# Performance work log

Hardware: AMD Instinct MI355X
Metric: run time of the kernel (lower is better)

Reference implementation:

```python
import jax, jax.numpy as jnp
import numpy as np
from jax import lax

EPS = 1e-10

def _ln(x, g, b):
    m = x.mean(-1, keepdims=True)
    v = x.var(-1, keepdims=True)
    return (x - m) / jnp.sqrt(v + 1e-5) * g + b

def _gather(t, idx):
    # t: (B, HW, c), idx: (B, HW, d) -> (B, HW, d, c); out[n,i,k,:] = t[n, idx[n,i,k], :]
    return jax.vmap(lambda tn, In: tn[In])(t, idx)

def setup_inputs() -> dict:
    key = jax.random.key(0)
    ks = jax.random.split(key, 20)
    b, v, c, d, h, w, hid, ksz = 2, 2, 128, 64, 64, 64, 256, 5
    hw = h * w
    Bf = b * v  # v_1 == 1 target view per reference view
    std = 0.02
    return {
        'features_mv': jax.random.normal(ks[0], (b, v, c, h, w), jnp.float32),
        'warp_indices': jax.random.randint(ks[1], (Bf, hw, d), 0, hw, jnp.int32),
        'depth_prob': jax.random.uniform(ks[2], (Bf, hw, d), jnp.float32),
        'ln1_g': jnp.ones((c,), jnp.float32), 'ln1_b': jnp.zeros((c,), jnp.float32),
        'wq': jax.random.normal(ks[3], (c, c), jnp.float32) * std, 'bq': jnp.zeros((c,), jnp.float32),
        'wk': jax.random.normal(ks[4], (c, c), jnp.float32) * std, 'bk': jnp.zeros((c,), jnp.float32),
        'wv': jax.random.normal(ks[5], (c, c), jnp.float32) * std, 'bv': jnp.zeros((c,), jnp.float32),
        'k_pe': jax.random.normal(ks[6], (1, 1, d), jnp.float32) * std,
        'v_pe': jax.random.normal(ks[7], (1, 1, d), jnp.float32) * std,
        'rpe': jax.random.normal(ks[8], (1, 1, d), jnp.float32) * std,
        'proj_w': jax.random.normal(ks[9], (c, c), jnp.float32) * std, 'proj_b': jnp.zeros((c,), jnp.float32),
        'ln2_g': jnp.ones((c,), jnp.float32), 'ln2_b': jnp.zeros((c,), jnp.float32),
        'fc1_w': jax.random.normal(ks[10], (c, hid), jnp.float32) * std, 'fc1_b': jnp.zeros((hid,), jnp.float32),
        'dw_w': jax.random.normal(ks[11], (hid, 1, ksz, ksz), jnp.float32) * std, 'dw_b': jnp.zeros((hid,), jnp.float32),
        'fc2_w': jax.random.normal(ks[12], (hid, c), jnp.float32) * std, 'fc2_b': jnp.zeros((c,), jnp.float32),
    }

def reference(features_mv, warp_indices, depth_prob, ln1_g, ln1_b, wq, bq, wk, bk, wv, bv,
              k_pe, v_pe, rpe, proj_w, proj_b, ln2_g, ln2_b, fc1_w, fc1_b, dw_w, dw_b, fc2_w, fc2_b):
    b, v, c, h, w = features_mv.shape
    hw = h * w
    hid = fc1_w.shape[1]
    scale = c ** (-0.5)  # num_heads = 1 -> head_dim = dim

    # (b v) (h w) c
    x = features_mv.reshape(b * v, c, hw).transpose(0, 2, 1)
    shortcut = x
    xn = _ln(x, ln1_g, ln1_b)
    q = xn @ wq + bq
    k = xn @ wk + bk
    vv = xn @ wv + bv

    # nn pairing: v=2, v_1=1 -> each reference view attends the other view
    Q = (q.reshape(b, v, hw, c) * scale).reshape(b * v, hw, c)
    K = k.reshape(b, v, hw, c)[:, ::-1].reshape(b * v, hw, c)
    V = vv.reshape(b, v, hw, c)[:, ::-1].reshape(b * v, hw, c)

    # SMM_QmK: cost[n,i,k] = sum_c Q[n,i,c] * K[n, idx[n,i,k], c]
    Kg = _gather(K, warp_indices)                       # (B, hw, d, c)
    cost = jnp.einsum('bic,bikc->bik', Q, Kg)
    Q_pe = Q.sum(-1, keepdims=True)                     # (B, hw, 1)
    cost = cost + Q_pe * k_pe + rpe                     # broadcast (1,1,d)

    # (Sim_UNet similarity refinement omitted: UNetModel source unavailable; identity here)
    attn = jax.nn.softmax(cost, axis=-1)
    attn = attn * depth_prob
    attn = (attn + EPS) / (attn.sum(-1, keepdims=True) + EPS)

    # SMM_AmV: out[n,i,c] = sum_k attn[n,i,k] * V[n, idx[n,i,k], c]
    Vg = _gather(V, warp_indices)                       # (B, hw, d, c)
    out = jnp.einsum('bik,bikc->bic', attn, Vg)
    out = out + (attn * v_pe).sum(-1, keepdims=True)

    # projection + residual (v_1 == 1 so B == b*v)
    x = shortcut + (out @ proj_w + proj_b)

    # ConvFFN residual branch
    xn2 = _ln(x, ln2_g, ln2_b)
    y = jax.nn.gelu(xn2 @ fc1_w + fc1_b, approximate=False)
    yi = y.transpose(0, 2, 1).reshape(b * v, hid, h, w)
    yc = lax.conv_general_dilated(yi, dw_w, (1, 1), 'SAME', feature_group_count=hid,
                                  dimension_numbers=('NCHW', 'OIHW', 'NCHW'))
    yc = jax.nn.gelu(yc + dw_b[None, :, None, None], approximate=False)
    y = y + yc.reshape(b * v, hid, hw).transpose(0, 2, 1)
    y = y @ fc2_w + fc2_b
    return x + y
```

## Files before the change

### kernel.cpp

```cpp
#include <hip/hip_runtime.h>
#include <math.h>

#define TOK   16384
#define HW    4096
#define C     128
#define D     64
#define HID   256

constexpr float LN_EPS = 1e-5f;
constexpr float EPS_R  = 1e-10f;
constexpr float QSCALE = 0.08838834764831845f;

typedef __attribute__((ext_vector_type(8))) short  bf16x8;
typedef __attribute__((ext_vector_type(4))) float  f32x4;
typedef __attribute__((ext_vector_type(2))) _Float16 half2v;
#define MFMA16(a, b, c) __builtin_amdgcn_mfma_f32_16x16x32_bf16((a), (b), (c), 0, 0, 0)

__device__ __forceinline__ float bflo(unsigned u) { return __uint_as_float(u << 16); }
__device__ __forceinline__ float bfhi(unsigned u) { return __uint_as_float(u & 0xffff0000u); }
__device__ __forceinline__ float bfu(unsigned short u) { return __uint_as_float((unsigned)u << 16); }
__device__ __forceinline__ unsigned short f2bf(float f) {
  unsigned u = __float_as_uint(f);
  unsigned r = (u + 0x7fffu + ((u >> 16) & 1u)) >> 16;
  return (unsigned short)r;
}
__device__ __forceinline__ unsigned short f2h(float f) {
  _Float16 h = (_Float16)f;
  unsigned short r;
  __builtin_memcpy(&r, &h, 2);
  return r;
}
__device__ __forceinline__ float gelu_exact(float x) {
  return 0.5f * x * (1.0f + erff(x * 0.7071067811865476f));
}

union U4H { uint4 v; half2v h[4]; };
union U1H { unsigned v; half2v h; };

#if __has_builtin(__builtin_amdgcn_fdot2)
__device__ __forceinline__ float dot2h(half2v a, half2v b, float c) {
  return __builtin_amdgcn_fdot2(a, b, c, false);
}
#else
__device__ __forceinline__ float dot2h(half2v a, half2v b, float c) {
  return c + (float)a.x * (float)b.x + (float)a.y * (float)b.y;
}
#endif

__global__ __launch_bounds__(256) void k_prepln1(const float* __restrict__ wq,
    const float* __restrict__ wk, const float* __restrict__ wv,
    const float* __restrict__ pw, const float* __restrict__ f1w,
    const float* __restrict__ f2w, unsigned short* __restrict__ wt,
    const float* __restrict__ feat, const float* __restrict__ g,
    const float* __restrict__ b, unsigned short* __restrict__ xnb) {
  __shared__ float tile[32][C + 1];
  int bidx = blockIdx.x;
  if (bidx < 512) {
    int id = bidx * 256 + threadIdx.x;
    if (id < 16384) {
      int n = id >> 7, k = id & 127;
      wt[id] = f2bf(wq[k * 128 + n]);
    } else if (id < 32768) {
      int e = id - 16384; int n = e >> 7, k = e & 127;
      wt[id] = f2bf(wk[k * 128 + n]);
    } else if (id < 49152) {
      int e = id - 32768; int n = e >> 7, k = e & 127;
      wt[id] = f2bf(wv[k * 128 + n]);
    } else if (id < 65536) {
      int e = id - 49152; int n = e >> 7, k = e & 127;
      wt[id] = f2bf(pw[k * 128 + n]);
    } else if (id < 98304) {
      int e = id - 65536; int n = e >> 7, k = e & 127;
      wt[id] = f2bf(f1w[k * 256 + n]);
    } else {
      int e = id - 98304; int n = e >> 8, k = e & 255;
      wt[id] = f2bf(f2w[k * 128 + n]);
    }
    return;
  }
  int t0 = (bidx - 512) * 32;
  int n = t0 / HW, i0 = t0 % HW;
  int tid = threadIdx.x;
  const float* fb = feat + (size_t)n * C * HW;
  for (int e = tid; e < 32 * C; e += 256) {
    int ch = e >> 5, ii = e & 31;
    tile[ii][ch] = fb[(size_t)ch * HW + i0 + ii];
  }
  __syncthreads();
  int wave = tid >> 6, lane = tid & 63;
  for (int tkn = wave; tkn < 32; tkn += 4) {
    float a0 = tile[tkn][lane];
    float a1 = tile[tkn][lane + 64];
    float s = a0 + a1;
    for (int off = 32; off; off >>= 1) s += __shfl_xor(s, off, 64);
    float mean = s * (1.0f / 128.0f);
    float d0 = a0 - mean, d1 = a1 - mean;
    float v = d0 * d0 + d1 * d1;
    for (int off = 32; off; off >>= 1) v += __shfl_xor(v, off, 64);
    float rstd = rsqrtf(v * (1.0f / 128.0f) + LN_EPS);
    size_t ro = (size_t)(t0 + tkn) * C;
    xnb[ro + lane]      = f2bf(d0 * rstd * g[lane] + b[lane]);
    xnb[ro + lane + 64] = f2bf(d1 * rstd * g[lane + 64] + b[lane + 64]);
  }
}

__global__ __launch_bounds__(256) void k_qkv(const unsigned short* __restrict__ xnb,
    const unsigned short* __restrict__ wt,
    const float* __restrict__ bq, const float* __restrict__ bk,
    const float* __restrict__ bv, unsigned short* __restrict__ qh,
    unsigned short* __restrict__ ksw, unsigned short* __restrict__ vsw) {
  int w = threadIdx.x >> 6, lane = threadIdx.x & 63;
  int q4 = lane >> 4, m = lane & 15;
  int t0 = blockIdx.x * 64 + w * 16;
  int wsel = blockIdx.y >> 1;
  int hf = blockIdx.y & 1;
  const unsigned short* Wt = wt + wsel * 16384;
  const unsigned short* ap = xnb + (size_t)(t0 + m) * C + q4 * 8;
  bf16x8 a[4];
  #pragma unroll
  for (int ks = 0; ks < 4; ks++) a[ks] = *(const bf16x8*)(ap + ks * 32);
  f32x4 acc[4];
  #pragma unroll
  for (int nt = 0; nt < 4; nt++) acc[nt] = (f32x4){0.f, 0.f, 0.f, 0.f};
  #pragma unroll
  for (int nt = 0; nt < 4; nt++) {
    const unsigned short* bp = Wt + (size_t)(hf * 64 + nt * 16 + m) * C + q4 * 8;
    #pragma unroll
    for (int ks = 0; ks < 4; ks++) {
      bf16x8 bfrag = *(const bf16x8*)(bp + ks * 32);
      acc[nt] = MFMA16(a[ks], bfrag, acc[nt]);
    }
  }
  const float* B = (wsel == 0) ? bq : ((wsel == 1) ? bk : bv);
  float sc = (wsel == 0) ? QSCALE : 1.0f;
  unsigned short* O = (wsel == 0) ? qh : ((wsel == 1) ? ksw : vsw);
  int n = t0 >> 12, i0 = t0 & 4095;
  int base = (wsel == 0) ? t0 : (((n ^ 1) << 12) + i0);
  #pragma unroll
  for (int nt = 0; nt < 4; nt++) {
    int col = hf * 64 + nt * 16 + m;
    float bb = B[col];
    #pragma unroll
    for (int reg = 0; reg < 4; reg++) {
      int row = base + q4 * 4 + reg;
      O[(size_t)row * C + col] = f2h((acc[nt][reg] + bb) * sc);
    }
  }
}

__global__ __launch_bounds__(256) void k_attn(const unsigned short* __restrict__ qh,
    const unsigned short* __restrict__ ksw, const unsigned short* __restrict__ vsw,
    const int* __restrict__ widx, const float* __restrict__ dprob,
    const float* __restrict__ kpe, const float* __restrict__ vpe,
    const float* __restrict__ rpe, unsigned short* __restrict__ aoutb) {
  int lane = threadIdx.x & 63;
  int wave = threadIdx.x >> 6;
  int bid = blockIdx.x;
  int n = (bid >> 1) & 3;
  int within = ((bid >> 3) << 1) | (bid & 1);
  int token = n * HW + within * 4 + wave;
  const unsigned short* Kb = ksw + (size_t)n * HW * C;
  const unsigned short* Vb = vsw + (size_t)n * HW * C;
  int g = lane >> 3, s = lane & 7;
  int myidx = widx[(size_t)token * D + lane];
  float mydp = dprob[(size_t)token * D + lane];
  half2v qreg[8];
  {
    const unsigned short* qp = qh + (size_t)token * C + s * 16;
    U4H qa, qb2;
    qa.v = *(const uint4*)(qp);
    qb2.v = *(const uint4*)(qp + 8);
    #pragma unroll
    for (int i = 0; i < 4; i++) { qreg[i] = qa.h[i]; qreg[4 + i] = qb2.h[i]; }
  }
  half2v ones = {(_Float16)1.0f, (_Float16)1.0f};
  float qpe = 0.f;
  #pragma unroll
  for (int i = 0; i < 8; i++) qpe = dot2h(qreg[i], ones, qpe);
  qpe += __shfl_xor(qpe, 1, 64);
  qpe += __shfl_xor(qpe, 2, 64);
  qpe += __shfl_xor(qpe, 4, 64);
  int rowv[8];
  #pragma unroll
  for (int pass = 0; pass < 8; ++pass)
    rowv[pass] = __shfl(myidx, pass * 8 + g, 64);
  uint4 ka[8], kb[8];
  #pragma unroll
  for (int pass = 0; pass < 8; ++pass) {
    const unsigned short* kr = Kb + (size_t)rowv[pass] * C + s * 16;
    ka[pass] = *(const uint4*)(kr);
    kb[pass] = *(const uint4*)(kr + 8);
  }
  float mycost = 0.f;
  #pragma unroll
  for (int pass = 0; pass < 8; ++pass) {
    U4H ua, ub;
    ua.v = ka[pass]; ub.v = kb[pass];
    float p = 0.f;
    #pragma unroll
    for (int i = 0; i < 4; i++) p = dot2h(ua.h[i], qreg[i], p);
    #pragma unroll
    for (int i = 0; i < 4; i++) p = dot2h(ub.h[i], qreg[4 + i], p);
    p += __shfl_xor(p, 1, 64);
    p += __shfl_xor(p, 2, 64);
    p += __shfl_xor(p, 4, 64);
    float t = __shfl(p, (lane & 7) << 3, 64);
    if (pass == g) mycost = t;
  }
  mycost += qpe * kpe[lane] + rpe[lane];
  float mx = mycost;
  for (int off = 32; off; off >>= 1) mx = fmaxf(mx, __shfl_xor(mx, off, 64));
  float e = __expf(mycost - mx);
  float ssum = e;
  for (int off = 32; off; off >>= 1) ssum += __shfl_xor(ssum, off, 64);
  float attn = (e / ssum) * mydp;
  float s2 = attn;
  for (int off = 32; off; off >>= 1) s2 += __shfl_xor(s2, off, 64);
  attn = (attn + EPS_R) / (s2 + EPS_R);
  float vpt = attn * vpe[lane];
  for (int off = 32; off; off >>= 1) vpt += __shfl_xor(vpt, off, 64);
  float o0 = vpt, o1 = vpt;
  unsigned att_u = __float_as_uint(attn);
  #pragma unroll
  for (int blk = 0; blk < 4; ++blk) {
    unsigned vv[16];
    #pragma unroll
    for (int j = 0; j < 16; j++) {
      int row = __builtin_amdgcn_readlane(myidx, blk * 16 + j);
      vv[j] = *(const unsigned*)(Vb + (size_t)row * C + lane * 2);
    }
    #pragma unroll
    for (int j = 0; j < 16; j++) {
      float a = __uint_as_float(__builtin_amdgcn_readlane(att_u, blk * 16 + j));
      U1H h; h.v = vv[j];
      o0 += a * (float)h.h.x;
      o1 += a * (float)h.h.y;
    }
  }
  unsigned pk = (unsigned)f2bf(o0) | ((unsigned)f2bf(o1) << 16);
  *(unsigned*)(aoutb + (size_t)token * C + lane * 2) = pk;
}

__global__ __launch_bounds__(256) void k_projfc1(
    const unsigned short* __restrict__ aoutb, const unsigned short* __restrict__ wt,
    const float* __restrict__ pb, const float* __restrict__ feat,
    float* __restrict__ xio, const float* __restrict__ g2,
    const float* __restrict__ b2, const float* __restrict__ f1b,
    unsigned short* __restrict__ y) {
  __shared__ unsigned short axn[16 * C];
  __shared__ float ps1[4][16];
  __shared__ float ps2[4][16];
  int lane = threadIdx.x & 63;
  int wave = threadIdx.x >> 6;
  int T0 = blockIdx.x * 16;
  int n = T0 >> 12;
  int q4 = lane >> 4, m = lane & 15;

  const unsigned short* ap = aoutb + (size_t)(T0 + m) * C + q4 * 8;
  bf16x8 a[4];
  #pragma unroll
  for (int ks = 0; ks < 4; ks++) a[ks] = *(const bf16x8*)(ap + ks * 32);
  const unsigned short* Wp = wt + 3 * 16384;
  f32x4 acc[2];
  #pragma unroll
  for (int nt = 0; nt < 2; nt++) acc[nt] = (f32x4){0.f, 0.f, 0.f, 0.f};
  #pragma unroll
  for (int nt = 0; nt < 2; nt++) {
    int colt = wave * 32 + nt * 16;
    const unsigned short* bp = Wp + (size_t)(colt + m) * C + q4 * 8;
    #pragma unroll
    for (int ks = 0; ks < 4; ks++) {
      bf16x8 bfrag = *(const bf16x8*)(bp + ks * 32);
      acc[nt] = MFMA16(a[ks], bfrag, acc[nt]);
    }
  }
  int ibase = (T0 & 4095) + q4 * 4;
  float s1[4] = {0.f, 0.f, 0.f, 0.f}, s2[4] = {0.f, 0.f, 0.f, 0.f};
  #pragma unroll
  for (int nt = 0; nt < 2; nt++) {
    int col = wave * 32 + nt * 16 + m;
    float bb = pb[col];
    const float* fp = feat + ((size_t)n * C + col) * HW + ibase;
    #pragma unroll
    for (int reg = 0; reg < 4; reg++) {
      float v = acc[nt][reg] + bb + fp[reg];
      acc[nt][reg] = v;
      s1[reg] += v;
      s2[reg] += v * v;
    }
  }
  #pragma unroll
  for (int reg = 0; reg < 4; reg++) {
    #pragma unroll
    for (int off = 1; off < 16; off <<= 1) {
      s1[reg] += __shfl_xor(s1[reg], off, 64);
      s2[reg] += __shfl_xor(s2[reg], off, 64);
    }
  }
  if (m == 0) {
    #pragma unroll
    for (int reg = 0; reg < 4; reg++) {
      ps1[wave][q4 * 4 + reg] = s1[reg];
      ps2[wave][q4 * 4 + reg] = s2[reg];
    }
  }
  __syncthreads();
  float mean[4], rstd[4];
  #pragma unroll
  for (int reg = 0; reg < 4; reg++) {
    int row = q4 * 4 + reg;
    float t1 = ps1[0][row] + ps1[1][row] + ps1[2][row] + ps1[3][row];
    float t2 = ps2[0][row] + ps2[1][row] + ps2[2][row] + ps2[3][row];
    mean[reg] = t1 * (1.0f / 128.0f);
    float var = t2 * (1.0f / 128.0f) - mean[reg] * mean[reg];
    rstd[reg] = rsqrtf(var + LN_EPS);
  }
  #pragma unroll
  for (int nt = 0; nt < 2; nt++) {
    int col = wave * 32 + nt * 16 + m;
    float gc = g2[col], bc = b2[col];
    #pragma unroll
    for (int reg = 0; reg < 4; reg++) {
      int row = q4 * 4 + reg;
      float v = acc[nt][reg];
      xio[(size_t)(T0 + row) * C + col] = v;
      unsigned short xv = f2bf((v - mean[reg]) * rstd[reg] * gc + bc);
      int boff = row * 256 + col * 2;
      boff ^= (row & 15) << 4;
      *(unsigned short*)((char*)axn + boff) = xv;
    }
  }
  __syncthreads();

  bf16x8 af[4];
  #pragma unroll
  for (int ks = 0; ks < 4; ks++) {
    int boff = m * 256 + ks * 64 + q4 * 16;
    boff ^= m << 4;
    af[ks] = *(const bf16x8*)((char*)axn + boff);
  }
  const unsigned short* Wf = wt + 65536;
  f32x4 acc2[4];
  #pragma unroll
  for (int nt = 0; nt < 4; nt++) acc2[nt] = (f32x4){0.f, 0.f, 0.f, 0.f};
  #pragma unroll
  for (int nt = 0; nt < 4; nt++) {
    int colt = wave * 64 + nt * 16;
    const unsigned short* bp = Wf + (size_t)(colt + m) * C + q4 * 8;
    #pragma unroll
    for (int ks = 0; ks < 4; ks++) {
      bf16x8 bfrag = *(const bf16x8*)(bp + ks * 32);
      acc2[nt] = MFMA16(af[ks], bfrag, acc2[nt]);
    }
  }
  #pragma unroll
  for (int nt = 0; nt < 4; nt++) {
    int col = wave * 64 + nt * 16 + m;
    float bb = f1b[col];
    #pragma unroll
    for (int reg = 0; reg < 4; reg++) {
      int row = T0 + q4 * 4 + reg;
      y[(size_t)row * HID + col] = f2bf(gelu_exact(acc2[nt][reg] + bb));
    }
  }
}

__global__ __launch_bounds__(256) void k_dwconv(const unsigned short* __restrict__ y,
    const float* __restrict__ w, const float* __restrict__ bias,
    unsigned short* __restrict__ ysum) {
  __shared__ float tile[8][401];
  __shared__ float wl[8][25];
  __shared__ float bl[8];
  __shared__ unsigned short outl[256][8];
  int bid = blockIdx.x;
  int tile_id = bid & 15;
  int cb = (bid >> 4) & 31;
  int n = bid >> 9;
  int ty = (tile_id >> 2) * 16, tx = (tile_id & 3) * 16;
  int ch0 = cb * 8;
  int tid = threadIdx.x;
  if (tid < 200) wl[tid / 25][tid % 25] = w[(size_t)(ch0 + tid / 25) * 25 + tid % 25];
  if (tid < 8) bl[tid] = bias[ch0 + tid];
  const unsigned short* yb = y + (size_t)n * HW * HID;
  for (int p = tid; p < 400; p += 256) {
    int py = p / 20, px = p % 20;
    int gy = ty + py - 2, gx = tx + px - 2;
    uint4 v = make_uint4(0u, 0u, 0u, 0u);
    if (gy >= 0 && gy < 64 && gx >= 0 && gx < 64)
      v = *(const uint4*)(yb + (size_t)(gy * 64 + gx) * HID + ch0);
    tile[0][p] = bflo(v.x); tile[1][p] = bfhi(v.x);
    tile[2][p] = bflo(v.y); tile[3][p] = bfhi(v.y);
    tile[4][p] = bflo(v.z); tile[5][p] = bfhi(v.z);
    tile[6][p] = bflo(v.w); tile[7][p] = bfhi(v.w);
  }
  __syncthreads();
  int cc = tid & 7;
  int xx = (tid >> 3) & 15;
  int yg = tid >> 7;
  float wreg[25];
  #pragma unroll
  for (int k = 0; k < 25; k++) wreg[k] = wl[cc][k];
  float bb = bl[cc];
  float win[12][5];
  #pragma unroll
  for (int r = 0; r < 12; r++)
    #pragma unroll
    for (int dx = 0; dx < 5; dx++)
      win[r][dx] = tile[cc][(yg * 8 + r) * 20 + xx + dx];
  #pragma unroll
  for (int j = 0; j < 8; ++j) {
    float acc = 0.f;
    #pragma unroll
    for (int dy = 0; dy < 5; ++dy)
      #pragma unroll
      for (int dx = 0; dx < 5; ++dx)
        acc += wreg[dy * 5 + dx] * win[j + dy][dx];
    float o = win[j + 2][2] + gelu_exact(acc + bb);
    int yy = yg * 8 + j;
    outl[yy * 16 + xx][cc] = f2bf(o);
  }
  __syncthreads();
  {
    int p = tid;
    int yy = p >> 4, xx2 = p & 15;
    uint4 val = *(const uint4*)outl[p];
    *(uint4*)(ysum + (size_t)(n * HW + (ty + yy) * 64 + tx + xx2) * HID + ch0) = val;
  }
}

__global__ __launch_bounds__(256) void k_fc2(const unsigned short* __restrict__ ysum,
    const unsigned short* __restrict__ wt, const float* __restrict__ f2b,
    const float* __restrict__ xio, float* __restrict__ outp) {
  int w = threadIdx.x >> 6, lane = threadIdx.x & 63;
  int q4 = lane >> 4, m = lane & 15;
  int t0 = blockIdx.x * 64 + w * 16;
  int quarter = blockIdx.y;
  const unsigned short* Wt = wt + 98304;
  const unsigned short* ap = ysum + (size_t)(t0 + m) * HID + q4 * 8;
  bf16x8 a[8];
  #pragma unroll
  for (int ks = 0; ks < 8; ks++) a[ks] = *(const bf16x8*)(ap + ks * 32);
  f32x4 acc[2];
  #pragma unroll
  for (int nt = 0; nt < 2; nt++) acc[nt] = (f32x4){0.f, 0.f, 0.f, 0.f};
  #pragma unroll
  for (int nt = 0; nt < 2; nt++) {
    const unsigned short* bp = Wt + (size_t)(quarter * 32 + nt * 16 + m) * HID + q4 * 8;
    #pragma unroll
    for (int ks = 0; ks < 8; ks++) {
      bf16x8 bfrag = *(const bf16x8*)(bp + ks * 32);
      acc[nt] = MFMA16(a[ks], bfrag, acc[nt]);
    }
  }
  #pragma unroll
  for (int nt = 0; nt < 2; nt++) {
    int col = quarter * 32 + nt * 16 + m;
    float bb = f2b[col];
    #pragma unroll
    for (int reg = 0; reg < 4; reg++) {
      int row = t0 + q4 * 4 + reg;
      outp[(size_t)row * C + col] = acc[nt][reg] + bb + xio[(size_t)row * C + col];
    }
  }
}

extern "C" void kernel_launch(void* const* d_in, const int* in_sizes, int n_in,
                              void* d_out, int out_size, void* d_ws, size_t ws_size,
                              hipStream_t stream) {
  (void)in_sizes; (void)n_in; (void)out_size; (void)ws_size;
  const float* feat  = (const float*)d_in[0];
  const int*   widx  = (const int*)d_in[1];
  const float* dprob = (const float*)d_in[2];
  const float* ln1g  = (const float*)d_in[3];
  const float* ln1b  = (const float*)d_in[4];
  const float* wq    = (const float*)d_in[5];
  const float* bq    = (const float*)d_in[6];
  const float* wk    = (const float*)d_in[7];
  const float* bk    = (const float*)d_in[8];
  const float* wv    = (const float*)d_in[9];
  const float* bv    = (const float*)d_in[10];
  const float* kpe   = (const float*)d_in[11];
  const float* vpe   = (const float*)d_in[12];
  const float* rpe   = (const float*)d_in[13];
  const float* pw    = (const float*)d_in[14];
  const float* pb    = (const float*)d_in[15];
  const float* ln2g  = (const float*)d_in[16];
  const float* ln2b  = (const float*)d_in[17];
  const float* f1w   = (const float*)d_in[18];
  const float* f1b   = (const float*)d_in[19];
  const float* dww   = (const float*)d_in[20];
  const float* dwb   = (const float*)d_in[21];
  const float* f2w   = (const float*)d_in[22];
  const float* f2b   = (const float*)d_in[23];

  float* ws = (float*)d_ws;
  const size_t M2 = (size_t)TOK * C;
  float* xio = ws;
  unsigned short* qhb   = (unsigned short*)(ws + M2);
  unsigned short* xnb   = (unsigned short*)(ws + M2 + M2 / 2);
  unsigned short* ksb   = (unsigned short*)(ws + 2 * M2);
  unsigned short* vsb   = (unsigned short*)(ws + 2 * M2 + M2 / 2);
  unsigned short* aoutb = (unsigned short*)(ws + 3 * M2);
  unsigned short* yb    = (unsigned short*)(ws + 3 * M2 + M2 / 2);
  unsigned short* ysumb = (unsigned short*)(ws + 4 * M2 + M2 / 2);
  unsigned short* wtb   = (unsigned short*)(ws + 5 * M2 + M2 / 2);

  k_prepln1<<<1024, 256, 0, stream>>>(wq, wk, wv, pw, f1w, f2w, wtb,
                                      feat, ln1g, ln1b, xnb);
  k_qkv    <<<dim3(TOK / 64, 6), 256, 0, stream>>>(xnb, wtb, bq, bk, bv, qhb, ksb, vsb);
  k_attn   <<<TOK / 4, 256, 0, stream>>>(qhb, ksb, vsb, widx, dprob, kpe, vpe, rpe, aoutb);
  k_projfc1<<<TOK / 16, 256, 0, stream>>>(aoutb, wtb, pb, feat, xio, ln2g, ln2b, f1b, yb);
  k_dwconv <<<2048, 256, 0, stream>>>(yb, dww, dwb, ysumb);
  k_fc2    <<<dim3(TOK / 64, 4), 256, 0, stream>>>(ysumb, wtb, f2b, xio, (float*)d_out);
}
```

Measured before the change: 205.4 us.

## Fuse six kernels into one persistent megakernel with hierarchical grid barriers

Replaces the six separate launches (LN1/weight prep, QKV, attention, proj+fc1, dwconv, fc2) with a single persistent kernel of 1024 blocks that runs each stage in sequence, separated by a two-level atomic grid barrier. The aim is to remove per-launch overhead and inter-kernel gaps. Each stage's work is redistributed over the fixed grid, so QKV now computes all three matrices per block and attention processes four tokens per wave. The risks are spin-wait barrier cost, deadlock if not all 1024 blocks are co-resident, and lower parallelism in stages that used larger grids before.

```diff
diff --git a/kernel.cpp b/kernel.cpp
--- a/kernel.cpp
+++ b/kernel.cpp
@@ -6,6 +6,7 @@
 #define C     128
 #define D     64
 #define HID   256
+#define NB    1024
 
 constexpr float LN_EPS = 1e-5f;
 constexpr float EPS_R  = 1e-10f;
@@ -18,7 +19,6 @@
 
 __device__ __forceinline__ float bflo(unsigned u) { return __uint_as_float(u << 16); }
 __device__ __forceinline__ float bfhi(unsigned u) { return __uint_as_float(u & 0xffff0000u); }
-__device__ __forceinline__ float bfu(unsigned short u) { return __uint_as_float((unsigned)u << 16); }
 __device__ __forceinline__ unsigned short f2bf(float f) {
   unsigned u = __float_as_uint(f);
   unsigned r = (u + 0x7fffu + ((u >> 16) & 1u)) >> 16;
@@ -47,419 +47,439 @@
 }
 #endif
 
-__global__ __launch_bounds__(256) void k_prepln1(const float* __restrict__ wq,
-    const float* __restrict__ wk, const float* __restrict__ wv,
-    const float* __restrict__ pw, const float* __restrict__ f1w,
-    const float* __restrict__ f2w, unsigned short* __restrict__ wt,
-    const float* __restrict__ feat, const float* __restrict__ g,
-    const float* __restrict__ b, unsigned short* __restrict__ xnb) {
-  __shared__ float tile[32][C + 1];
-  int bidx = blockIdx.x;
-  if (bidx < 512) {
-    int id = bidx * 256 + threadIdx.x;
-    if (id < 16384) {
-      int n = id >> 7, k = id & 127;
-      wt[id] = f2bf(wq[k * 128 + n]);
-    } else if (id < 32768) {
-      int e = id - 16384; int n = e >> 7, k = e & 127;
-      wt[id] = f2bf(wk[k * 128 + n]);
-    } else if (id < 49152) {
-      int e = id - 32768; int n = e >> 7, k = e & 127;
-      wt[id] = f2bf(wv[k * 128 + n]);
-    } else if (id < 65536) {
-      int e = id - 49152; int n = e >> 7, k = e & 127;
-      wt[id] = f2bf(pw[k * 128 + n]);
-    } else if (id < 98304) {
-      int e = id - 65536; int n = e >> 7, k = e & 127;
-      wt[id] = f2bf(f1w[k * 256 + n]);
-    } else {
-      int e = id - 98304; int n = e >> 8, k = e & 255;
-      wt[id] = f2bf(f2w[k * 128 + n]);
-    }
-    return;
-  }
-  int t0 = (bidx - 512) * 32;
-  int n = t0 / HW, i0 = t0 % HW;
+__device__ __forceinline__ void grid_barrier(unsigned* bar, int idx) {
+  __syncthreads();
+  if (threadIdx.x == 0) {
+    unsigned* reg0 = bar + idx * 1024;
+    unsigned* root = reg0;
+    unsigned* leaf = reg0 + 16 + ((blockIdx.x >> 5) << 4);
+    unsigned p = __hip_atomic_fetch_add(leaf, 1u, __ATOMIC_ACQ_REL,
+                                        __HIP_MEMORY_SCOPE_AGENT);
+    if (p == 31u)
+      __hip_atomic_fetch_add(root, 1u, __ATOMIC_ACQ_REL,
+                             __HIP_MEMORY_SCOPE_AGENT);
+    while (__hip_atomic_load(root, __ATOMIC_ACQUIRE,
+                             __HIP_MEMORY_SCOPE_AGENT) < 32u)
+      __builtin_amdgcn_s_sleep(2);
+  }
+  __syncthreads();
+}
+
+__global__ __launch_bounds__(256, 4) void k_mega(
+    const float* __restrict__ feat, const int* __restrict__ widx,
+    const float* __restrict__ dprob, const float* __restrict__ ln1g,
+    const float* __restrict__ ln1b, const float* __restrict__ wq,
+    const float* __restrict__ bq, const float* __restrict__ wk,
+    const float* __restrict__ bk, const float* __restrict__ wv,
+    const float* __restrict__ bv, const float* __restrict__ kpe,
+    const float* __restrict__ vpe, const float* __restrict__ rpe,
+    const float* __restrict__ pw, const float* __restrict__ pb,
+    const float* __restrict__ ln2g, const float* __restrict__ ln2b,
+    const float* __restrict__ f1w, const float* __restrict__ f1b,
+    const float* __restrict__ dww, const float* __restrict__ dwb,
+    const float* __restrict__ f2w, const float* __restrict__ f2b,
+    float* __restrict__ xio, unsigned short* __restrict__ qhb,
+    unsigned short* __restrict__ xnb, unsigned short* __restrict__ ksb,
+    unsigned short* __restrict__ vsb, unsigned short* __restrict__ aoutb,
+    unsigned short* __restrict__ yb, unsigned short* __restrict__ ysumb,
+    unsigned short* __restrict__ wtb, unsigned* __restrict__ bar,
+    float* __restrict__ outp) {
+  __shared__ __align__(16) char smem[17760];
   int tid = threadIdx.x;
-  const float* fb = feat + (size_t)n * C * HW;
-  for (int e = tid; e < 32 * C; e += 256) {
-    int ch = e >> 5, ii = e & 31;
-    tile[ii][ch] = fb[(size_t)ch * HW + i0 + ii];
-  }
-  __syncthreads();
-  int wave = tid >> 6, lane = tid & 63;
-  for (int tkn = wave; tkn < 32; tkn += 4) {
-    float a0 = tile[tkn][lane];
-    float a1 = tile[tkn][lane + 64];
-    float s = a0 + a1;
-    for (int off = 32; off; off >>= 1) s += __shfl_xor(s, off, 64);
-    float mean = s * (1.0f / 128.0f);
-    float d0 = a0 - mean, d1 = a1 - mean;
-    float v = d0 * d0 + d1 * d1;
-    for (int off = 32; off; off >>= 1) v += __shfl_xor(v, off, 64);
-    float rstd = rsqrtf(v * (1.0f / 128.0f) + LN_EPS);
-    size_t ro = (size_t)(t0 + tkn) * C;
-    xnb[ro + lane]      = f2bf(d0 * rstd * g[lane] + b[lane]);
-    xnb[ro + lane + 64] = f2bf(d1 * rstd * g[lane + 64] + b[lane + 64]);
-  }
-}
-
-__global__ __launch_bounds__(256) void k_qkv(const unsigned short* __restrict__ xnb,
-    const unsigned short* __restrict__ wt,
-    const float* __restrict__ bq, const float* __restrict__ bk,
-    const float* __restrict__ bv, unsigned short* __restrict__ qh,
-    unsigned short* __restrict__ ksw, unsigned short* __restrict__ vsw) {
-  int w = threadIdx.x >> 6, lane = threadIdx.x & 63;
-  int q4 = lane >> 4, m = lane & 15;
-  int t0 = blockIdx.x * 64 + w * 16;
-  int wsel = blockIdx.y >> 1;
-  int hf = blockIdx.y & 1;
-  const unsigned short* Wt = wt + wsel * 16384;
-  const unsigned short* ap = xnb + (size_t)(t0 + m) * C + q4 * 8;
-  bf16x8 a[4];
-  #pragma unroll
-  for (int ks = 0; ks < 4; ks++) a[ks] = *(const bf16x8*)(ap + ks * 32);
-  f32x4 acc[4];
-  #pragma unroll
-  for (int nt = 0; nt < 4; nt++) acc[nt] = (f32x4){0.f, 0.f, 0.f, 0.f};
-  #pragma unroll
-  for (int nt = 0; nt < 4; nt++) {
-    const unsigned short* bp = Wt + (size_t)(hf * 64 + nt * 16 + m) * C + q4 * 8;
-    #pragma unroll
-    for (int ks = 0; ks < 4; ks++) {
-      bf16x8 bfrag = *(const bf16x8*)(bp + ks * 32);
-      acc[nt] = MFMA16(a[ks], bfrag, acc[nt]);
-    }
-  }
-  const float* B = (wsel == 0) ? bq : ((wsel == 1) ? bk : bv);
-  float sc = (wsel == 0) ? QSCALE : 1.0f;
-  unsigned short* O = (wsel == 0) ? qh : ((wsel == 1) ? ksw : vsw);
-  int n = t0 >> 12, i0 = t0 & 4095;
-  int base = (wsel == 0) ? t0 : (((n ^ 1) << 12) + i0);
-  #pragma unroll
-  for (int nt = 0; nt < 4; nt++) {
-    int col = hf * 64 + nt * 16 + m;
-    float bb = B[col];
+  int lane = tid & 63;
+  int wave = tid >> 6;
+  int b = blockIdx.x;
+
+  {
+    float* t16 = (float*)smem;
+    int t0 = b * 16;
+    int nv = t0 >> 12, i0 = t0 & 4095;
+    const float* fb = feat + (size_t)nv * C * HW;
+    for (int e = tid; e < 16 * C; e += 256) {
+      int ch = e >> 4, ii = e & 15;
+      t16[ii * 129 + ch] = fb[(size_t)ch * HW + i0 + ii];
+    }
+    if (tid < 128) {
+      int id = b * 128 + tid;
+      if (id < 16384) {
+        int n = id >> 7, k = id & 127;
+        wtb[id] = f2bf(wq[k * 128 + n]);
+      } else if (id < 32768) {
+        int e = id - 16384; int n = e >> 7, k = e & 127;
+        wtb[id] = f2bf(wk[k * 128 + n]);
+      } else if (id < 49152) {
+        int e = id - 32768; int n = e >> 7, k = e & 127;
+        wtb[id] = f2bf(wv[k * 128 + n]);
+      } else if (id < 65536) {
+        int e = id - 49152; int n = e >> 7, k = e & 127;
+        wtb[id] = f2bf(pw[k * 128 + n]);
+      } else if (id < 98304) {
+        int e = id - 65536; int n = e >> 7, k = e & 127;
+        wtb[id] = f2bf(f1w[k * 256 + n]);
+      } else {
+        int e = id - 98304; int n = e >> 8, k = e & 255;
+        wtb[id] = f2bf(f2w[k * 128 + n]);
+      }
+    }
+    __syncthreads();
+    for (int tkn = wave; tkn < 16; tkn += 4) {
+      float a0 = t16[tkn * 129 + lane];
+      float a1 = t16[tkn * 129 + lane + 64];
+      float s = a0 + a1;
+      for (int off = 32; off; off >>= 1) s += __shfl_xor(s, off, 64);
+      float mean = s * (1.0f / 128.0f);
+      float d0 = a0 - mean, d1 = a1 - mean;
+      float v = d0 * d0 + d1 * d1;
+      for (int off = 32; off; off >>= 1) v += __shfl_xor(v, off, 64);
+      float rstd = rsqrtf(v * (1.0f / 128.0f) + LN_EPS);
+      size_t ro = (size_t)(t0 + tkn) * C;
+      xnb[ro + lane]      = f2bf(d0 * rstd * ln1g[lane] + ln1b[lane]);
+      xnb[ro + lane + 64] = f2bf(d1 * rstd * ln1g[lane + 64] + ln1b[lane + 64]);
+    }
+  }
+  grid_barrier(bar, 0);
+
+  {
+    int t0 = b * 16;
+    int q4 = lane >> 4, m = lane & 15;
+    const unsigned short* ap = xnb + (size_t)(t0 + m) * C + q4 * 8;
+    bf16x8 a[4];
+    #pragma unroll
+    for (int ks = 0; ks < 4; ks++) a[ks] = *(const bf16x8*)(ap + ks * 32);
+    int nv = t0 >> 12, i0 = t0 & 4095;
+    int swbase = ((nv ^ 1) << 12) + i0;
+    #pragma unroll
+    for (int mat = 0; mat < 3; ++mat) {
+      const unsigned short* Wt = wtb + mat * 16384;
+      f32x4 acc[2];
+      #pragma unroll
+      for (int nt = 0; nt < 2; nt++) acc[nt] = (f32x4){0.f, 0.f, 0.f, 0.f};
+      #pragma unroll
+      for (int nt = 0; nt < 2; nt++) {
+        int colt = wave * 32 + nt * 16;
+        const unsigned short* bp = Wt + (size_t)(colt + m) * C + q4 * 8;
+        #pragma unroll
+        for (int ks = 0; ks < 4; ks++) {
+          bf16x8 bfrag = *(const bf16x8*)(bp + ks * 32);
+          acc[nt] = MFMA16(a[ks], bfrag, acc[nt]);
+        }
+      }
+      const float* B = (mat == 0) ? bq : ((mat == 1) ? bk : bv);
+      float sc = (mat == 0) ? QSCALE : 1.0f;
+      unsigned short* O = (mat == 0) ? qhb : ((mat == 1) ? ksb : vsb);
+      int base = (mat == 0) ? t0 : swbase;
+      #pragma unroll
+      for (int nt = 0; nt < 2; nt++) {
+        int col = wave * 32 + nt * 16 + m;
+        float bb = B[col];
+        #pragma unroll
+        for (int reg = 0; reg < 4; reg++) {
+          int row = base + q4 * 4 + reg;
+          O[(size_t)row * C + col] = f2h((acc[nt][reg] + bb) * sc);
+        }
+      }
+    }
+  }
+  grid_barrier(bar, 1);
+
+  {
+    int nv = (b & 7) >> 1;
+    int u = ((b >> 3) << 1) | (b & 1);
+    const unsigned short* Kb = ksb + (size_t)nv * HW * C;
+    const unsigned short* Vb = vsb + (size_t)nv * HW * C;
+    int gq = lane >> 3, sq = lane & 7;
+    half2v ones = {(_Float16)1.0f, (_Float16)1.0f};
+    for (int tj = 0; tj < 4; ++tj) {
+      int token = nv * HW + u * 16 + wave * 4 + tj;
+      int myidx = widx[(size_t)token * D + lane];
+      float mydp = dprob[(size_t)token * D + lane];
+      half2v qreg[8];
+      {
+        const unsigned short* qp = qhb + (size_t)token * C + sq * 16;
+        U4H qa, qb2;
+        qa.v = *(const uint4*)(qp);
+        qb2.v = *(const uint4*)(qp + 8);
+        #pragma unroll
+        for (int i = 0; i < 4; i++) { qreg[i] = qa.h[i]; qreg[4 + i] = qb2.h[i]; }
+      }
+      float qpe = 0.f;
+      #pragma unroll
+      for (int i = 0; i < 8; i++) qpe = dot2h(qreg[i], ones, qpe);
+      qpe += __shfl_xor(qpe, 1, 64);
+      qpe += __shfl_xor(qpe, 2, 64);
+      qpe += __shfl_xor(qpe, 4, 64);
+      int rowv[8];
+      #pragma unroll
+      for (int pass = 0; pass < 8; ++pass)
+        rowv[pass] = __shfl(myidx, pass * 8 + gq, 64);
+      uint4 ka[8], kb2[8];
+      #pragma unroll
+      for (int pass = 0; pass < 8; ++pass) {
+        const unsigned short* kr = Kb + (size_t)rowv[pass] * C + sq * 16;
+        ka[pass] = *(const uint4*)(kr);
+        kb2[pass] = *(const uint4*)(kr + 8);
+      }
+      float mycost = 0.f;
+      #pragma unroll
+      for (int pass = 0; pass < 8; ++pass) {
+        U4H ua, ub;
+        ua.v = ka[pass]; ub.v = kb2[pass];
+        float p = 0.f;
+        #pragma unroll
+        for (int i = 0; i < 4; i++) p = dot2h(ua.h[i], qreg[i], p);
+        #pragma unroll
+        for (int i = 0; i < 4; i++) p = dot2h(ub.h[i], qreg[4 + i], p);
+        p += __shfl_xor(p, 1, 64);
+        p += __shfl_xor(p, 2, 64);
+        p += __shfl_xor(p, 4, 64);
+        float t = __shfl(p, (lane & 7) << 3, 64);
+        if (pass == gq) mycost = t;
+      }
+      mycost += qpe * kpe[lane] + rpe[lane];
+      float mx = mycost;
+      for (int off = 32; off; off >>= 1) mx = fmaxf(mx, __shfl_xor(mx, off, 64));
+      float e = __expf(mycost - mx);
+      float ssum = e;
+      for (int off = 32; off; off >>= 1) ssum += __shfl_xor(ssum, off, 64);
+      float attn = (e / ssum) * mydp;
+      float s2 = attn;
+      for (int off = 32; off; off >>= 1) s2 += __shfl_xor(s2, off, 64);
+      attn = (attn + EPS_R) / (s2 + EPS_R);
+      float vpt = attn * vpe[lane];
+      for (int off = 32; off; off >>= 1) vpt += __shfl_xor(vpt, off, 64);
+      float o0 = vpt, o1 = vpt;
+      unsigned att_u = __float_as_uint(attn);
+      #pragma unroll
+      for (int blk = 0; blk < 4; ++blk) {
+        unsigned vv[16];
+        #pragma unroll
+        for (int j = 0; j < 16; j++) {
+          int row = __builtin_amdgcn_readlane(myidx, blk * 16 + j);
+          vv[j] = *(const unsigned*)(Vb + (size_t)row * C + lane * 2);
+        }
+        #pragma unroll
+        for (int j = 0; j < 16; j++) {
+          float a = __uint_as_float(__builtin_amdgcn_readlane(att_u, blk * 16 + j));
+          U1H h; h.v = vv[j];
+          o0 += a * (float)h.h.x;
+          o1 += a * (float)h.h.y;
+        }
+      }
+      unsigned pk = (unsigned)f2bf(o0) | ((unsigned)f2bf(o1) << 16);
+      *(unsigned*)(aoutb + (size_t)token * C + lane * 2) = pk;
+    }
+  }
+  grid_barrier(bar, 2);
+
+  {
+    unsigned short* axn = (unsigned short*)smem;
+    float* ps1 = (float*)(smem + 4096);
+    float* ps2 = (float*)(smem + 4352);
+    int T0 = b * 16;
+    int nv = T0 >> 12;
+    int q4 = lane >> 4, m = lane & 15;
+    const unsigned short* ap = aoutb + (size_t)(T0 + m) * C + q4 * 8;
+    bf16x8 a[4];
+    #pragma unroll
+    for (int ks = 0; ks < 4; ks++) a[ks] = *(const bf16x8*)(ap + ks * 32);
+    const unsigned short* Wp = wtb + 3 * 16384;
+    f32x4 acc[2];
+    #pragma unroll
+    for (int nt = 0; nt < 2; nt++) acc[nt] = (f32x4){0.f, 0.f, 0.f, 0.f};
+    #pragma unroll
+    for (int nt = 0; nt < 2; nt++) {
+      int colt = wave * 32 + nt * 16;
+      const unsigned short* bp = Wp + (size_t)(colt + m) * C + q4 * 8;
+      #pragma unroll
+      for (int ks = 0; ks < 4; ks++) {
+        bf16x8 bfrag = *(const bf16x8*)(bp + ks * 32);
+        acc[nt] = MFMA16(a[ks], bfrag, acc[nt]);
+      }
+    }
+    int ibase = (T0 & 4095) + q4 * 4;
+    float s1[4] = {0.f, 0.f, 0.f, 0.f}, s2[4] = {0.f, 0.f, 0.f, 0.f};
+    #pragma unroll
+    for (int nt = 0; nt < 2; nt++) {
+      int col = wave * 32 + nt * 16 + m;
+      float bb = pb[col];
+      const float* fp = feat + ((size_t)nv * C + col) * HW + ibase;
+      #pragma unroll
+      for (int reg = 0; reg < 4; reg++) {
+        float v = acc[nt][reg] + bb + fp[reg];
+        acc[nt][reg] = v;
+        s1[reg] += v;
+        s2[reg] += v * v;
+      }
+    }
     #pragma unroll
     for (int reg = 0; reg < 4; reg++) {
-      int row = base + q4 * 4 + reg;
-      O[(size_t)row * C + col] = f2h((acc[nt][reg] + bb) * sc);
-    }
-  }
-}
-
-__global__ __launch_bounds__(256) void k_attn(const unsigned short* __restrict__ qh,
-    const unsigned short* __restrict__ ksw, const unsigned short* __restrict__ vsw,
-    const int* __restrict__ widx, const float* __restrict__ dprob,
-    const float* __restrict__ kpe, const float* __restrict__ vpe,
-    const float* __restrict__ rpe, unsigned short* __restrict__ aoutb) {
-  int lane = threadIdx.x & 63;
-  int wave = threadIdx.x >> 6;
-  int bid = blockIdx.x;
-  int n = (bid >> 1) & 3;
-  int within = ((bid >> 3) << 1) | (bid & 1);
-  int token = n * HW + within * 4 + wave;
-  const unsigned short* Kb = ksw + (size_t)n * HW * C;
-  const unsigned short* Vb = vsw + (size_t)n * HW * C;
-  int g = lane >> 3, s = lane & 7;
-  int myidx = widx[(size_t)token * D + lane];
-  float mydp = dprob[(size_t)token * D + lane];
-  half2v qreg[8];
-  {
-    const unsigned short* qp = qh + (size_t)token * C + s * 16;
-    U4H qa, qb2;
-    qa.v = *(const uint4*)(qp);
-    qb2.v = *(const uint4*)(qp + 8);
-    #pragma unroll
-    for (int i = 0; i < 4; i++) { qreg[i] = qa.h[i]; qreg[4 + i] = qb2.h[i]; }
-  }
-  half2v ones = {(_Float16)1.0f, (_Float16)1.0f};
-  float qpe = 0.f;
-  #pragma unroll
-  for (int i = 0; i < 8; i++) qpe = dot2h(qreg[i], ones, qpe);
-  qpe += __shfl_xor(qpe, 1, 64);
-  qpe += __shfl_xor(qpe, 2, 64);
-  qpe += __shfl_xor(qpe, 4, 64);
-  int rowv[8];
-  #pragma unroll
-  for (int pass = 0; pass < 8; ++pass)
-    rowv[pass] = __shfl(myidx, pass * 8 + g, 64);
-  uint4 ka[8], kb[8];
-  #pragma unroll
-  for (int pass = 0; pass < 8; ++pass) {
-    const unsigned short* kr = Kb + (size_t)rowv[pass] * C + s * 16;
-    ka[pass] = *(const uint4*)(kr);
-    kb[pass] = *(const uint4*)(kr + 8);
-  }
-  float mycost = 0.f;
-  #pragma unroll
-  for (int pass = 0; pass < 8; ++pass) {
-    U4H ua, ub;
-    ua.v = ka[pass]; ub.v = kb[pass];
-    float p = 0.f;
-    #pragma unroll
-    for (int i = 0; i < 4; i++) p = dot2h(ua.h[i], qreg[i], p);
-    #pragma unroll
-    for (int i = 0; i < 4; i++) p = dot2h(ub.h[i], qreg[4 + i], p);
-    p += __shfl_xor(p, 1, 64);
-    p += __shfl_xor(p, 2, 64);
-    p += __shfl_xor(p, 4, 64);
-    float t = __shfl(p, (lane & 7) << 3, 64);
-    if (pass == g) mycost = t;
-  }
-  mycost += qpe * kpe[lane] + rpe[lane];
-  float mx = mycost;
-  for (int off = 32; off; off >>= 1) mx = fmaxf(mx, __shfl_xor(mx, off, 64));
-  float e = __expf(mycost - mx);
-  float ssum = e;
-  for (int off = 32; off; off >>= 1) ssum += __shfl_xor(ssum, off, 64);
-  float attn = (e / ssum) * mydp;
-  float s2 = attn;
-  for (int off = 32; off; off >>= 1) s2 += __shfl_xor(s2, off, 64);
-  attn = (attn + EPS_R) / (s2 + EPS_R);
-  float vpt = attn * vpe[lane];
-  for (int off = 32; off; off >>= 1) vpt += __shfl_xor(vpt, off, 64);
-  float o0 = vpt, o1 = vpt;
-  unsigned att_u = __float_as_uint(attn);
-  #pragma unroll
-  for (int blk = 0; blk < 4; ++blk) {
-    unsigned vv[16];
-    #pragma unroll
-    for (int j = 0; j < 16; j++) {
-      int row = __builtin_amdgcn_readlane(myidx, blk * 16 + j);
-      vv[j] = *(const unsigned*)(Vb + (size_t)row * C + lane * 2);
-    }
-    #pragma unroll
-    for (int j = 0; j < 16; j++) {
-      float a = __uint_as_float(__builtin_amdgcn_readlane(att_u, blk * 16 + j));
-      U1H h; h.v = vv[j];
-      o0 += a * (float)h.h.x;
-      o1 += a * (float)h.h.y;
-    }
-  }
-  unsigned pk = (unsigned)f2bf(o0) | ((unsigned)f2bf(o1) << 16);
-  *(unsigned*)(aoutb + (size_t)token * C + lane * 2) = pk;
-}
-
-__global__ __launch_bounds__(256) void k_projfc1(
-    const unsigned short* __restrict__ aoutb, const unsigned short* __restrict__ wt,
-    const float* __restrict__ pb, const float* __restrict__ feat,
-    float* __restrict__ xio, const float* __restrict__ g2,
-    const float* __restrict__ b2, const float* __restrict__ f1b,
-    unsigned short* __restrict__ y) {
-  __shared__ unsigned short axn[16 * C];
-  __shared__ float ps1[4][16];
-  __shared__ float ps2[4][16];
-  int lane = threadIdx.x & 63;
-  int wave = threadIdx.x >> 6;
-  int T0 = blockIdx.x * 16;
-  int n = T0 >> 12;
-  int q4 = lane >> 4, m = lane & 15;
-
-  const unsigned short* ap = aoutb + (size_t)(T0 + m) * C + q4 * 8;
-  bf16x8 a[4];
-  #pragma unroll
-  for (int ks = 0; ks < 4; ks++) a[ks] = *(const bf16x8*)(ap + ks * 32);
-  const unsigned short* Wp = wt + 3 * 16384;
-  f32x4 acc[2];
-  #pragma unroll
-  for (int nt = 0; nt < 2; nt++) acc[nt] = (f32x4){0.f, 0.f, 0.f, 0.f};
-  #pragma unroll
-  for (int nt = 0; nt < 2; nt++) {
-    int colt = wave * 32 + nt * 16;
-    const unsigned short* bp = Wp + (size_t)(colt + m) * C + q4 * 8;
-    #pragma unroll
-    for (int ks = 0; ks < 4; ks++) {
-      bf16x8 bfrag = *(const bf16x8*)(bp + ks * 32);
-      acc[nt] = MFMA16(a[ks], bfrag, acc[nt]);
-    }
-  }
-  int ibase = (T0 & 4095) + q4 * 4;
-  float s1[4] = {0.f, 0.f, 0.f, 0.f}, s2[4] = {0.f, 0.f, 0.f, 0.f};
-  #pragma unroll
-  for (int nt = 0; nt < 2; nt++) {
-    int col = wave * 32 + nt * 16 + m;
-    float bb = pb[col];
-    const float* fp = feat + ((size_t)n * C + col) * HW + ibase;
-    #pragma unroll
-    for (int reg = 0; reg < 4; reg++) {
-      float v = acc[nt][reg] + bb + fp[reg];
-      acc[nt][reg] = v;
-      s1[reg] += v;
-      s2[reg] += v * v;
-    }
-  }
-  #pragma unroll
-  for (int reg = 0; reg < 4; reg++) {
-    #pragma unroll
-    for (int off = 1; off < 16; off <<= 1) {
-      s1[reg] += __shfl_xor(s1[reg], off, 64);
-      s2[reg] += __shfl_xor(s2[reg], off, 64);
-    }
-  }
-  if (m == 0) {
-    #pragma unroll
-    for (int reg = 0; reg < 4; reg++) {
-      ps1[wave][q4 * 4 + reg] = s1[reg];
-      ps2[wave][q4 * 4 + reg] = s2[reg];
-    }
-  }
-  __syncthreads();
-  float mean[4], rstd[4];
-  #pragma unroll
-  for (int reg = 0; reg < 4; reg++) {
-    int row = q4 * 4 + reg;
-    float t1 = ps1[0][row] + ps1[1][row] + ps1[2][row] + ps1[3][row];
-    float t2 = ps2[0][row] + ps2[1][row] + ps2[2][row] + ps2[3][row];
-    mean[reg] = t1 * (1.0f / 128.0f);
-    float var = t2 * (1.0f / 128.0f) - mean[reg] * mean[reg];
-    rstd[reg] = rsqrtf(var + LN_EPS);
-  }
-  #pragma unroll
-  for (int nt = 0; nt < 2; nt++) {
-    int col = wave * 32 + nt * 16 + m;
-    float gc = g2[col], bc = b2[col];
+      #pragma unroll
+      for (int off = 1; off < 16; off <<= 1) {
+        s1[reg] += __shfl_xor(s1[reg], off, 64);
+        s2[reg] += __shfl_xor(s2[reg], off, 64);
+      }
+    }
+    if (m == 0) {
+      #pragma unroll
+      for (int reg = 0; reg < 4; reg++) {
+        ps1[wave * 16 + q4 * 4 + reg] = s1[reg];
+        ps2[wave * 16 + q4 * 4 + reg] = s2[reg];
+      }
+    }
+    __syncthreads();
+    float mean[4], rstd[4];
     #pragma unroll
     for (int reg = 0; reg < 4; reg++) {
       int row = q4 * 4 + reg;
-      float v = acc[nt][reg];
-      xio[(size_t)(T0 + row) * C + col] = v;
-      unsigned short xv = f2bf((v - mean[reg]) * rstd[reg] * gc + bc);
-      int boff = row * 256 + col * 2;
-      boff ^= (row & 15) << 4;
-      *(unsigned short*)((char*)axn + boff) = xv;
-    }
-  }
-  __syncthreads();
-
-  bf16x8 af[4];
-  #pragma unroll
-  for (int ks = 0; ks < 4; ks++) {
-    int boff = m * 256 + ks * 64 + q4 * 16;
-    boff ^= m << 4;
-    af[ks] = *(const bf16x8*)((char*)axn + boff);
-  }
-  const unsigned short* Wf = wt + 65536;
-  f32x4 acc2[4];
-  #pragma unroll
-  for (int nt = 0; nt < 4; nt++) acc2[nt] = (f32x4){0.f, 0.f, 0.f, 0.f};
-  #pragma unroll
-  for (int nt = 0; nt < 4; nt++) {
-    int colt = wave * 64 + nt * 16;
-    const unsigned short* bp = Wf + (size_t)(colt + m) * C + q4 * 8;
+      float t1 = ps1[row] + ps1[16 + row] + ps1[32 + row] + ps1[48 + row];
+      float t2 = ps2[row] + ps2[16 + row] + ps2[32 + row] + ps2[48 + row];
+      mean[reg] = t1 * (1.0f / 128.0f);
+      float var = t2 * (1.0f / 128.0f) - mean[reg] * mean[reg];
+      rstd[reg] = rsqrtf(var + LN_EPS);
+    }
+    #pragma unroll
+    for (int nt = 0; nt < 2; nt++) {
+      int col = wave * 32 + nt * 16 + m;
+      float gc = ln2g[col], bc = ln2b[col];
+      #pragma unroll
+      for (int reg = 0; reg < 4; reg++) {
+        int row = q4 * 4 + reg;
+        float v = acc[nt][reg];
+        xio[(size_t)(T0 + row) * C + col] = v;
+        unsigned short xv = f2bf((v - mean[reg]) * rstd[reg] * gc + bc);
+        int boff = row * 256 + col * 2;
+        boff ^= (row & 15) << 4;
+        *(unsigned short*)(smem + boff) = xv;
+      }
+    }
+    __syncthreads();
+    bf16x8 af[4];
     #pragma unroll
     for (int ks = 0; ks < 4; ks++) {
-      bf16x8 bfrag = *(const bf16x8*)(bp + ks * 32);
-      acc2[nt] = MFMA16(af[ks], bfrag, acc2[nt]);
-    }
-  }
-  #pragma unroll
-  for (int nt = 0; nt < 4; nt++) {
-    int col = wave * 64 + nt * 16 + m;
-    float bb = f1b[col];
-    #pragma unroll
-    for (int reg = 0; reg < 4; reg++) {
-      int row = T0 + q4 * 4 + reg;
-      y[(size_t)row * HID + col] = f2bf(gelu_exact(acc2[nt][reg] + bb));
-    }
-  }
-}
-
-__global__ __launch_bounds__(256) void k_dwconv(const unsigned short* __restrict__ y,
-    const float* __restrict__ w, const float* __restrict__ bias,
-    unsigned short* __restrict__ ysum) {
-  __shared__ float tile[8][401];
-  __shared__ float wl[8][25];
-  __shared__ float bl[8];
-  __shared__ unsigned short outl[256][8];
-  int bid = blockIdx.x;
-  int tile_id = bid & 15;
-  int cb = (bid >> 4) & 31;
-  int n = bid >> 9;
-  int ty = (tile_id >> 2) * 16, tx = (tile_id & 3) * 16;
-  int ch0 = cb * 8;
-  int tid = threadIdx.x;
-  if (tid < 200) wl[tid / 25][tid % 25] = w[(size_t)(ch0 + tid / 25) * 25 + tid % 25];
-  if (tid < 8) bl[tid] = bias[ch0 + tid];
-  const unsigned short* yb = y + (size_t)n * HW * HID;
-  for (int p = tid; p < 400; p += 256) {
-    int py = p / 20, px = p % 20;
-    int gy = ty + py - 2, gx = tx + px - 2;
-    uint4 v = make_uint4(0u, 0u, 0u, 0u);
-    if (gy >= 0 && gy < 64 && gx >= 0 && gx < 64)
-      v = *(const uint4*)(yb + (size_t)(gy * 64 + gx) * HID + ch0);
-    tile[0][p] = bflo(v.x); tile[1][p] = bfhi(v.x);
-    tile[2][p] = bflo(v.y); tile[3][p] = bfhi(v.y);
-    tile[4][p] = bflo(v.z); tile[5][p] = bfhi(v.z);
-    tile[6][p] = bflo(v.w); tile[7][p] = bfhi(v.w);
-  }
-  __syncthreads();
-  int cc = tid & 7;
-  int xx = (tid >> 3) & 15;
-  int yg = tid >> 7;
-  float wreg[25];
-  #pragma unroll
-  for (int k = 0; k < 25; k++) wreg[k] = wl[cc][k];
-  float bb = bl[cc];
-  float win[12][5];
-  #pragma unroll
-  for (int r = 0; r < 12; r++)
-    #pragma unroll
-    for (int dx = 0; dx < 5; dx++)
-      win[r][dx] = tile[cc][(yg * 8 + r) * 20 + xx + dx];
-  #pragma unroll
-  for (int j = 0; j < 8; ++j) {
-    float acc = 0.f;
-    #pragma unroll
-    for (int dy = 0; dy < 5; ++dy)
-      #pragma unroll
-      for (int dx = 0; dx < 5; ++dx)
-        acc += wreg[dy * 5 + dx] * win[j + dy][dx];
-    float o = win[j + 2][2] + gelu_exact(acc + bb);
-    int yy = yg * 8 + j;
-    outl[yy * 16 + xx][cc] = f2bf(o);
-  }
-  __syncthreads();
+      int boff = m * 256 + ks * 64 + q4 * 16;
+      boff ^= m << 4;
+      af[ks] = *(const bf16x8*)(smem + boff);
+    }
+    const unsigned short* Wf = wtb + 65536;
+    f32x4 acc2[4];
+    #pragma unroll
+    for (int nt = 0; nt < 4; nt++) acc2[nt] = (f32x4){0.f, 0.f, 0.f, 0.f};
+    #pragma unroll
+    for (int nt = 0; nt < 4; nt++) {
+      int colt = wave * 64 + nt * 16;
+      const unsigned short* bp = Wf + (size_t)(colt + m) * C + q4 * 8;
+      #pragma unroll
+      for (int ks = 0; ks < 4; ks++) {
+        bf16x8 bfrag = *(const bf16x8*)(bp + ks * 32);
+        acc2[nt] = MFMA16(af[ks], bfrag, acc2[nt]);
+      }
+    }
+    #pragma unroll
+    for (int nt = 0; nt < 4; nt++) {
+      int col = wave * 64 + nt * 16 + m;
+      float bb = f1b[col];
+      #pragma unroll
+      for (int reg = 0; reg < 4; reg++) {
+        int row = T0 + q4 * 4 + reg;
+        yb[(size_t)row * HID + col] = f2bf(gelu_exact(acc2[nt][reg] + bb));
+      }
+    }
+  }
+  grid_barrier(bar, 3);
+
   {
-    int p = tid;
-    int yy = p >> 4, xx2 = p & 15;
-    uint4 val = *(const uint4*)outl[p];
-    *(uint4*)(ysum + (size_t)(n * HW + (ty + yy) * 64 + tx + xx2) * HID + ch0) = val;
-  }
-}
-
-__global__ __launch_bounds__(256) void k_fc2(const unsigned short* __restrict__ ysum,
-    const unsigned short* __restrict__ wt, const float* __restrict__ f2b,
-    const float* __restrict__ xio, float* __restrict__ outp) {
-  int w = threadIdx.x >> 6, lane = threadIdx.x & 63;
-  int q4 = lane >> 4, m = lane & 15;
-  int t0 = blockIdx.x * 64 + w * 16;
-  int quarter = blockIdx.y;
-  const unsigned short* Wt = wt + 98304;
-  const unsigned short* ap = ysum + (size_t)(t0 + m) * HID + q4 * 8;
-  bf16x8 a[8];
-  #pragma unroll
-  for (int ks = 0; ks < 8; ks++) a[ks] = *(const bf16x8*)(ap + ks * 32);
-  f32x4 acc[2];
-  #pragma unroll
-  for (int nt = 0; nt < 2; nt++) acc[nt] = (f32x4){0.f, 0.f, 0.f, 0.f};
-  #pragma unroll
-  for (int nt = 0; nt < 2; nt++) {
-    const unsigned short* bp = Wt + (size_t)(quarter * 32 + nt * 16 + m) * HID + q4 * 8;
-    #pragma unroll
-    for (int ks = 0; ks < 8; ks++) {
-      bf16x8 bfrag = *(const bf16x8*)(bp + ks * 32);
-      acc[nt] = MFMA16(a[ks], bfrag, acc[nt]);
-    }
-  }
-  #pragma unroll
-  for (int nt = 0; nt < 2; nt++) {
-    int col = quarter * 32 + nt * 16 + m;
-    float bb = f2b[col];
-    #pragma unroll
-    for (int reg = 0; reg < 4; reg++) {
-      int row = t0 + q4 * 4 + reg;
-      outp[(size_t)row * C + col] = acc[nt][reg] + bb + xio[(size_t)row * C + col];
+    float* tile = (float*)smem;
+    float* wl   = (float*)(smem + 12832);
+    float* bl   = (float*)(smem + 13632);
+    unsigned short* outl = (unsigned short*)(smem + 13664);
+    for (int u5 = b; u5 < 2048; u5 += NB) {
+      __syncthreads();
+      int tile_id = u5 & 15;
+      int cb = (u5 >> 4) & 31;
+      int nn = u5 >> 9;
+      int ty = (tile_id >> 2) * 16, tx = (tile_id & 3) * 16;
+      int ch0 = cb * 8;
+      if (tid < 200) wl[(tid / 25) * 25 + tid % 25] =
+          dww[(size_t)(ch0 + tid / 25) * 25 + tid % 25];
+      if (tid < 8) bl[tid] = dwb[ch0 + tid];
+      const unsigned short* ybp = yb + (size_t)nn * HW * HID;
+      for (int p = tid; p < 400; p += 256) {
+        int py = p / 20, px = p % 20;
+        int gy = ty + py - 2, gx = tx + px - 2;
+        uint4 v = make_uint4(0u, 0u, 0u, 0u);
+        if (gy >= 0 && gy < 64 && gx >= 0 && gx < 64)
+          v = *(const uint4*)(ybp + (size_t)(gy * 64 + gx) * HID + ch0);
+        tile[0 * 401 + p] = bflo(v.x); tile[1 * 401 + p] = bfhi(v.x);
+        tile[2 * 401 + p] = bflo(v.y); tile[3 * 401 + p] = bfhi(v.y);
+        tile[4 * 401 + p] = bflo(v.z); tile[5 * 401 + p] = bfhi(v.z);
+        tile[6 * 401 + p] = bflo(v.w); tile[7 * 401 + p] = bfhi(v.w);
+      }
+      __syncthreads();
+      int cc = tid & 7;
+      int xx = (tid >> 3) & 15;
+      int yg = tid >> 7;
+      float wreg[25];
+      #pragma unroll
+      for (int k = 0; k < 25; k++) wreg[k] = wl[cc * 25 + k];
+      float bb = bl[cc];
+      float win[12][5];
+      #pragma unroll
+      for (int r = 0; r < 12; r++)
+        #pragma unroll
+        for (int dx = 0; dx < 5; dx++)
+          win[r][dx] = tile[cc * 401 + (yg * 8 + r) * 20 + xx + dx];
+      #pragma unroll
+      for (int j = 0; j < 8; ++j) {
+        float acc = 0.f;
+        #pragma unroll
+        for (int dy = 0; dy < 5; ++dy)
+          #pragma unroll
+          for (int dx = 0; dx < 5; ++dx)
+            acc += wreg[dy * 5 + dx] * win[j + dy][dx];
+        float o = win[j + 2][2] + gelu_exact(acc + bb);
+        int yy = yg * 8 + j;
+        outl[(yy * 16 + xx) * 8 + cc] = f2bf(o);
+      }
+      __syncthreads();
+      {
+        int p = tid;
+        int yy = p >> 4, xx2 = p & 15;
+        uint4 val = *(const uint4*)(outl + p * 8);
+        *(uint4*)(ysumb + (size_t)(nn * HW + (ty + yy) * 64 + tx + xx2) * HID + ch0) = val;
+      }
+    }
+  }
+  grid_barrier(bar, 4);
+
+  {
+    int t0 = b * 16;
+    int q4 = lane >> 4, m = lane & 15;
+    const unsigned short* Wt = wtb + 98304;
+    const unsigned short* ap = ysumb + (size_t)(t0 + m) * HID + q4 * 8;
+    bf16x8 a[8];
+    #pragma unroll
+    for (int ks = 0; ks < 8; ks++) a[ks] = *(const bf16x8*)(ap + ks * 32);
+    f32x4 acc[2];
+    #pragma unroll
+    for (int nt = 0; nt < 2; nt++) acc[nt] = (f32x4){0.f, 0.f, 0.f, 0.f};
+    #pragma unroll
+    for (int nt = 0; nt < 2; nt++) {
+      const unsigned short* bp = Wt + (size_t)(wave * 32 + nt * 16 + m) * HID + q4 * 8;
+      #pragma unroll
+      for (int ks = 0; ks < 8; ks++) {
+        bf16x8 bfrag = *(const bf16x8*)(bp + ks * 32);
+        acc[nt] = MFMA16(a[ks], bfrag, acc[nt]);
+      }
+    }
+    #pragma unroll
+    for (int nt = 0; nt < 2; nt++) {
+      int col = wave * 32 + nt * 16 + m;
+      float bb = f2b[col];
+      #pragma unroll
+      for (int reg = 0; reg < 4; reg++) {
+        int row = t0 + q4 * 4 + reg;
+        outp[(size_t)row * C + col] = acc[nt][reg] + bb + xio[(size_t)row * C + col];
+      }
     }
   }
 }
@@ -504,12 +524,12 @@
   unsigned short* yb    = (unsigned short*)(ws + 3 * M2 + M2 / 2);
   unsigned short* ysumb = (unsigned short*)(ws + 4 * M2 + M2 / 2);
   unsigned short* wtb   = (unsigned short*)(ws + 5 * M2 + M2 / 2);
-
-  k_prepln1<<<1024, 256, 0, stream>>>(wq, wk, wv, pw, f1w, f2w, wtb,
-                                      feat, ln1g, ln1b, xnb);
-  k_qkv    <<<dim3(TOK / 64, 6), 256, 0, stream>>>(xnb, wtb, bq, bk, bv, qhb, ksb, vsb);
-  k_attn   <<<TOK / 4, 256, 0, stream>>>(qhb, ksb, vsb, widx, dprob, kpe, vpe, rpe, aoutb);
-  k_projfc1<<<TOK / 16, 256, 0, stream>>>(aoutb, wtb, pb, feat, xio, ln2g, ln2b, f1b, yb);
-  k_dwconv <<<2048, 256, 0, stream>>>(yb, dww, dwb, ysumb);
-  k_fc2    <<<dim3(TOK / 64, 4), 256, 0, stream>>>(ysumb, wtb, f2b, xio, (float*)d_out);
-}
+  unsigned* bar         = (unsigned*)(ws + 6 * M2);
+
+  hipMemsetAsync(bar, 0, 5 * 4096, stream);
+  k_mega<<<NB, 256, 0, stream>>>(feat, widx, dprob, ln1g, ln1b, wq, bq, wk, bk,
+                                 wv, bv, kpe, vpe, rpe, pw, pb, ln2g, ln2b,
+                                 f1w, f1b, dww, dwb, f2w, f2b,
+                                 xio, qhb, xnb, ksb, vsb, aoutb, yb, ysumb,
+                                 wtb, bar, (float*)d_out);
+}
```

Result: slower. 652.8 us (+217.8%).
